# Kernel optimization log

Measured on AMD Instinct MI355X. Metric: run time of the kernel, lower is better.

## Reference

```python
import jax, jax.numpy as jnp
import numpy as np

B, N, C = 1, 6400, 256
NUM_CAMS, NUM_HEADS, NUM_LEVELS, NUM_POINTS = 6, 8, 3, 8
LVL_SHAPES = [(64, 176), (32, 88), (16, 44)]
IMG_H, IMG_W = 512, 1408


def setup_inputs():
    key = jax.random.key(0)
    ks = jax.random.split(key, 16)
    # Gaussian means in ego frame: depth z in [2,40]; x/y scaled so projections land in-image
    z = jax.random.uniform(ks[0], (B, N, 1), minval=2.0, maxval=40.0)
    xy = jax.random.uniform(ks[1], (B, N, 2), minval=-0.5, maxval=0.5)
    means = jnp.concatenate([xy[..., 0:1] * z * 0.8, xy[..., 1:2] * z * 0.4, z], -1)
    feature = jax.random.normal(ks[2], (B, N, C)) * 0.5
    feat0 = jax.random.normal(ks[3], (B * NUM_CAMS, C, 64, 176)) * 0.5
    feat1 = jax.random.normal(ks[4], (B * NUM_CAMS, C, 32, 88)) * 0.5
    feat2 = jax.random.normal(ks[5], (B * NUM_CAMS, C, 16, 44)) * 0.5
    cam2ego = jnp.tile(jnp.eye(4), (B, NUM_CAMS, 1, 1))
    cam2ego = cam2ego.at[..., :3, 3].set(jax.random.uniform(ks[6], (B, NUM_CAMS, 3), minval=-0.5, maxval=0.5))
    intrins = jnp.tile(jnp.array([[500., 0., 704.], [0., 500., 256.], [0., 0., 1.]]), (B, NUM_CAMS, 1, 1))
    post_rots = jnp.tile(jnp.eye(3), (B, NUM_CAMS, 1, 1))
    post_trans = jnp.concatenate([jax.random.uniform(ks[7], (B, NUM_CAMS, 2), minval=-30., maxval=30.),
                                  jnp.zeros((B, NUM_CAMS, 1))], -1)
    # deformable-attn style bias init for sampling offsets (as in init_weights)
    thetas = np.arange(NUM_HEADS) * (2.0 * np.pi / NUM_HEADS)
    grid = np.stack([np.cos(thetas), np.sin(thetas)], -1)
    grid = grid / np.abs(grid).max(-1, keepdims=True)
    grid = np.tile(grid.reshape(NUM_HEADS, 1, 1, 2), (1, NUM_LEVELS, NUM_POINTS, 1))
    grid = grid * (np.arange(NUM_POINTS) + 1).reshape(1, 1, NUM_POINTS, 1)
    b_off = jnp.asarray(grid.reshape(-1), jnp.float32)
    W_off = jax.random.normal(ks[8], (C, NUM_HEADS * NUM_LEVELS * NUM_POINTS * 2)) * 0.01
    W_attn = jax.random.normal(ks[9], (C, NUM_HEADS * NUM_LEVELS * NUM_POINTS)) * 0.02
    b_attn = jnp.zeros((NUM_HEADS * NUM_LEVELS * NUM_POINTS,))
    W_val = jax.random.normal(ks[10], (C, C)) * (1.0 / np.sqrt(C))
    b_val = jnp.zeros((C,))
    W_out = jax.random.normal(ks[11], (C, C)) * (1.0 / np.sqrt(C))
    b_out = jnp.zeros((C,))
    cams_embeds = jax.random.normal(ks[12], (NUM_CAMS, C))
    level_embeds = jax.random.normal(ks[13], (NUM_LEVELS, C))
    ln_g = jnp.ones((C,))
    ln_b = jnp.zeros((C,))
    return dict(means=means, feature=feature, feat0=feat0, feat1=feat1, feat2=feat2,
                cam2ego=cam2ego, intrins=intrins, post_rots=post_rots, post_trans=post_trans,
                W_off=W_off, b_off=b_off, W_attn=W_attn, b_attn=b_attn, W_val=W_val, b_val=b_val,
                W_out=W_out, b_out=b_out, cams_embeds=cams_embeds, level_embeds=level_embeds,
                ln_g=ln_g, ln_b=ln_b, img_h=IMG_H, img_w=IMG_W)


def _msda(value, shapes, loc, attn):
    # Multi-scale deformable attention (matches multi_scale_deformable_attn_pytorch,
    # i.e. grid_sample bilinear, align_corners=False, zero padding).
    # value [Bc,S,H,D]; loc [Bc,Nq,H,L,P,2] in [0,1]; attn [Bc,Nq,H,L,P]
    Bc, S, Hh, D = value.shape
    Nq, P = loc.shape[1], loc.shape[4]
    out = jnp.zeros((Bc, Hh, Nq, D), value.dtype)
    start = 0
    for lvl, (h, w) in enumerate(shapes):
        v = value[:, start:start + h * w].transpose(0, 2, 1, 3)  # [Bc,H,h*w,D]
        l = loc[:, :, :, lvl]                                    # [Bc,Nq,H,P,2]
        x = l[..., 0] * w - 0.5  # align_corners=False pixel coords
        y = l[..., 1] * h - 0.5
        x0 = jnp.floor(x)
        y0 = jnp.floor(y)
        tx = x - x0
        ty = y - y0
        a = attn[:, :, :, lvl]                                   # [Bc,Nq,H,P]
        def samp(xi, yi, wgt):
            valid = (xi >= 0) & (xi <= w - 1) & (yi >= 0) & (yi <= h - 1)
            idx = (jnp.clip(yi, 0, h - 1) * w + jnp.clip(xi, 0, w - 1)).astype(jnp.int32)
            idx = idx.transpose(0, 2, 1, 3).reshape(Bc, Hh, Nq * P)
            g = jnp.take_along_axis(v, idx[..., None], axis=2)   # [Bc,H,Nq*P,D]
            coef = wgt * jnp.where(valid, 1.0, 0.0).astype(v.dtype) * a
            return g * coef.transpose(0, 2, 1, 3).reshape(Bc, Hh, Nq * P, 1)
        acc = (samp(x0, y0, (1 - tx) * (1 - ty)) + samp(x0 + 1, y0, tx * (1 - ty))
               + samp(x0, y0 + 1, (1 - tx) * ty) + samp(x0 + 1, y0 + 1, tx * ty))
        out = out + acc.reshape(Bc, Hh, Nq, P, D).sum(3)
        start += h * w
    return out.transpose(0, 2, 1, 3).reshape(Bc, Nq, Hh * D)


def reference(means, feature, feat0, feat1, feat2, cam2ego, intrins, post_rots, post_trans,
              W_off, b_off, W_attn, b_attn, W_val, b_val, W_out, b_out,
              cams_embeds, level_embeds, ln_g, ln_b, img_h, img_w):
    Bq, Nq, Cc = feature.shape
    D = Cc // NUM_HEADS
    # --- project reference points into each camera (project_reference_points) ---
    mh = jnp.concatenate([means, jnp.ones((Bq, Nq, 1), means.dtype)], -1)      # [B,N,4]
    means_cam = jnp.einsum('bcij,bnj->bcni', jnp.linalg.inv(cam2ego), mh)[..., :3]
    means_img = jnp.einsum('bcij,bcnj->bcni', intrins, means_cam)              # [B,cams,N,3]
    mi = jnp.concatenate([means_img[..., :2] / (means_img[..., 2:] + 1e-4), means_img[..., 2:]], -1)
    mi = jnp.einsum('bcij,bcnj->bcni', post_rots, mi) + post_trans[:, :, None, :]
    coor = mi[..., :2] / jnp.array([img_w, img_h], feature.dtype)              # [B,cams,N,2]
    depth = mi[..., 2]
    mask = ((depth > 0.01) & (coor[..., 0] > 0.) & (coor[..., 0] < 1.)
            & (coor[..., 1] > 0.) & (coor[..., 1] < 1.))                        # [B,cams,N]
    # --- per-query sampling offsets / attention weights (shared across cameras) ---
    offsets = (feature @ W_off + b_off).reshape(Bq, Nq, NUM_HEADS, NUM_LEVELS, NUM_POINTS, 2)
    attn = jax.nn.softmax((feature @ W_attn + b_attn).reshape(Bq, Nq, NUM_HEADS, NUM_LEVELS * NUM_POINTS), -1)
    attn = attn.reshape(Bq, Nq, NUM_HEADS, NUM_LEVELS, NUM_POINTS)
    # --- flatten multi-level feats + cam/level embeds, value projection ---
    feats = (feat0, feat1, feat2)
    shapes = [(f.shape[2], f.shape[3]) for f in feats]
    flat = []
    for lvl, f in enumerate(feats):
        h, w = shapes[lvl]
        fl = f.reshape(Bq, NUM_CAMS, Cc, h * w)
        fl = fl + cams_embeds[None, :, :, None] + level_embeds[lvl][None, None, :, None]
        flat.append(fl)
    value = jnp.concatenate(flat, -1).transpose(0, 1, 3, 2).reshape(Bq * NUM_CAMS, -1, Cc)
    value = (value @ W_val + b_val).reshape(Bq * NUM_CAMS, -1, NUM_HEADS, D)
    # --- sampling locations per camera ---
    norm = jnp.array([[w, h] for (h, w) in shapes], feature.dtype)             # [L,2] = (W_l,H_l)
    loc = coor[:, :, :, None, None, None, :] + offsets[:, None] / norm[None, None, None, None, :, None, :]
    loc = loc.reshape(Bq * NUM_CAMS, Nq, NUM_HEADS, NUM_LEVELS, NUM_POINTS, 2)
    attn_bc = jnp.broadcast_to(attn[:, None], (Bq, NUM_CAMS, Nq, NUM_HEADS, NUM_LEVELS, NUM_POINTS))
    attn_bc = attn_bc.reshape(Bq * NUM_CAMS, Nq, NUM_HEADS, NUM_LEVELS, NUM_POINTS)
    out = _msda(value, shapes, loc, attn_bc).reshape(Bq, NUM_CAMS, Nq, Cc)
    # --- mask-weighted combine over cameras (mathematically equals the rebatch/scatter) ---
    mf = mask.astype(feature.dtype)
    slots = (out * mf[..., None]).sum(1) / jnp.maximum(mf.sum(1), 1.0)[..., None]
    slots = slots @ W_out + b_out
    x = slots + feature  # dropout is identity at inference
    mu = jnp.mean(x, -1, keepdims=True)
    var = jnp.mean((x - mu) ** 2, -1, keepdims=True)
    return (x - mu) / jnp.sqrt(var + 1e-5) * ln_g + ln_b
```

## Files before the change

kernel.cpp:

```cpp
#include <hip/hip_runtime.h>
#include <hip/hip_bf16.h>

typedef __bf16 bf16;
typedef __attribute__((ext_vector_type(4))) float f32x4;
typedef __attribute__((ext_vector_type(8))) bf16 bf16x8;
typedef __attribute__((ext_vector_type(2))) bf16 bf16x2;

#define NCAMS 6
#define NQ 6400
#define CH 256
#define NH 8
#define NL 3
#define NP 8
#define S_TOT 14784

#if __has_builtin(__builtin_amdgcn_fdot2_f32_bf16) && __has_builtin(__builtin_amdgcn_perm)
#define MSDA_DOT2 1
#else
#define MSDA_DOT2 0
#endif

__global__ __launch_bounds__(256) void k_prep(
    const float* __restrict__ means, const float* __restrict__ cam2ego,
    const float* __restrict__ intrins, const float* __restrict__ post_rots,
    const float* __restrict__ post_trans, const int* __restrict__ img_h,
    const int* __restrict__ img_w,
    const float* __restrict__ W_val, const float* __restrict__ W_off,
    const float* __restrict__ W_attn, const float* __restrict__ W_out,
    float* __restrict__ coor, float* __restrict__ maskf,
    bf16* __restrict__ Wvp, bf16* __restrict__ Woap, bf16* __restrict__ Wop)
{
    int bid = blockIdx.x;
    if (bid < 150) {
        int idx = bid * 256 + threadIdx.x;
        if (idx >= NCAMS * NQ) return;
        int cam = idx / NQ, n = idx % NQ;
        float mx = means[n*3+0], my = means[n*3+1], mz = means[n*3+2];
        const float* M = cam2ego + cam*16;
        float R[3][3], t[3];
        #pragma unroll
        for (int r = 0; r < 3; r++) {
            #pragma unroll
            for (int c = 0; c < 3; c++) R[r][c] = M[r*4+c];
            t[r] = M[r*4+3];
        }
        float dx = mx - t[0], dy = my - t[1], dz = mz - t[2];
        float xc = R[0][0]*dx + R[1][0]*dy + R[2][0]*dz;
        float yc = R[0][1]*dx + R[1][1]*dy + R[2][1]*dz;
        float zc = R[0][2]*dx + R[1][2]*dy + R[2][2]*dz;
        const float* K = intrins + cam*9;
        float ix = K[0]*xc + K[1]*yc + K[2]*zc;
        float iy = K[3]*xc + K[4]*yc + K[5]*zc;
        float iz = K[6]*xc + K[7]*yc + K[8]*zc;
        float px = ix / (iz + 1e-4f), py = iy / (iz + 1e-4f), pz = iz;
        const float* P = post_rots + cam*9;
        const float* T = post_trans + cam*3;
        float vx = P[0]*px + P[1]*py + P[2]*pz + T[0];
        float vy = P[3]*px + P[4]*py + P[5]*pz + T[1];
        float vz = P[6]*px + P[7]*py + P[8]*pz + T[2];
        float cx = vx / (float)img_w[0];
        float cy = vy / (float)img_h[0];
        bool ok = (vz > 0.01f) && (cx > 0.f) && (cx < 1.f) && (cy > 0.f) && (cy < 1.f);
        coor[idx*2+0] = cx;
        coor[idx*2+1] = cy;
        maskf[idx] = ok ? 1.f : 0.f;
        return;
    }
    int flat = (bid - 150) * 256 + threadIdx.x;
    if (flat < 8192) {
        int kc = flat >> 10, rem = flat & 1023;
        int nf = rem >> 6, lane = rem & 63;
        int q = lane >> 4, col = nf*16 + (lane & 15);
        bf16x8 v;
        #pragma unroll
        for (int j = 0; j < 8; j++) v[j] = (bf16)W_val[(size_t)(kc*32 + q*8 + j)*256 + col];
        *reinterpret_cast<bf16x8*>(Wvp + (size_t)flat*8) = v;
    } else if (flat < 26624) {
        int f2 = flat - 8192;
        int kc = f2 / (36*64), rem = f2 % (36*64);
        int nf = rem >> 6, lane = rem & 63;
        int q = lane >> 4, col = nf*16 + (lane & 15);
        bf16x8 v;
        #pragma unroll
        for (int j = 0; j < 8; j++) {
            int k = kc*32 + q*8 + j;
            float x = (col < 384) ? W_off[(size_t)k*384 + col] : W_attn[(size_t)k*192 + (col-384)];
            v[j] = (bf16)x;
        }
        *reinterpret_cast<bf16x8*>(Woap + (size_t)f2*8) = v;
    } else if (flat < 34816) {
        int f3 = flat - 26624;
        int kc = f3 >> 10, rem = f3 & 1023;
        int nf = rem >> 6, lane = rem & 63;
        int q = lane >> 4, col = nf*16 + (lane & 15);
        bf16x8 v;
        #pragma unroll
        for (int j = 0; j < 8; j++) v[j] = (bf16)W_out[(size_t)(kc*32 + q*8 + j)*256 + col];
        *reinterpret_cast<bf16x8*>(Wop + (size_t)f3*8) = v;
    }
}

__global__ __launch_bounds__(256) void k_offattn2(
    const float* __restrict__ feature, const bf16* __restrict__ Woap,
    const float* __restrict__ b_off, const float* __restrict__ b_attn,
    float* __restrict__ offs, bf16* __restrict__ attn_out)
{
    __shared__ float lg[16][200];
    int t = threadIdx.x, lane = t & 63, w = t >> 6;
    int q = lane >> 4, r16 = lane & 15;
    int n0 = blockIdx.x * 16;

    f32x4 acc[9];
    #pragma unroll
    for (int i = 0; i < 9; i++) acc[i] = (f32x4){0.f,0.f,0.f,0.f};

    const float* arow = feature + (size_t)(n0 + r16)*CH;
    for (int kc = 0; kc < 8; kc++) {
        f32x4 a0 = *reinterpret_cast<const f32x4*>(arow + kc*32 + q*8);
        f32x4 a1 = *reinterpret_cast<const f32x4*>(arow + kc*32 + q*8 + 4);
        bf16x8 afr;
        #pragma unroll
        for (int i = 0; i < 4; i++) { afr[i] = (bf16)a0[i]; afr[4+i] = (bf16)a1[i]; }
        #pragma unroll
        for (int nf9 = 0; nf9 < 9; nf9++) {
            bf16x8 bfr = *reinterpret_cast<const bf16x8*>(Woap + ((size_t)(kc*36 + w*9 + nf9)*64 + lane)*8);
            acc[nf9] = __builtin_amdgcn_mfma_f32_16x16x32_bf16(afr, bfr, acc[nf9], 0, 0, 0);
        }
    }
    #pragma unroll
    for (int nf9 = 0; nf9 < 9; nf9++) {
        int nfg = w*9 + nf9;
        int nglob = nfg*16 + r16;
        if (nfg < 24) {
            float bias = b_off[nglob];
            #pragma unroll
            for (int r = 0; r < 4; r++)
                offs[(size_t)(n0 + q*4 + r)*384 + nglob] = acc[nf9][r] + bias;
        } else {
            int la = nglob - 384;
            float bias = b_attn[la];
            #pragma unroll
            for (int r = 0; r < 4; r++)
                lg[q*4 + r][la] = acc[nf9][r] + bias;
        }
    }
    __syncthreads();
    if (t < 128) {
        int m = t >> 3, h = t & 7;
        const float* L = &lg[m][h*24];
        float mx = -1e30f;
        #pragma unroll
        for (int j = 0; j < 24; j++) mx = fmaxf(mx, L[j]);
        float e[24]; float s = 0.f;
        #pragma unroll
        for (int j = 0; j < 24; j++) { e[j] = __expf(L[j] - mx); s += e[j]; }
        float inv = 1.f / s;
        #pragma unroll
        for (int j = 0; j < 24; j++) attn_out[(size_t)(n0+m)*192 + h*24 + j] = (bf16)(e[j]*inv);
    }
}

__global__ __launch_bounds__(256) void k_valproj(
    const float* __restrict__ f0, const float* __restrict__ f1, const float* __restrict__ f2,
    const float* __restrict__ cams_embeds, const float* __restrict__ level_embeds,
    const bf16* __restrict__ Wvp, const float* __restrict__ b_val, bf16* __restrict__ value)
{
    __shared__ alignas(16) bf16 A[64][48];
    __shared__ alignas(16) bf16 Cst[16][256];
    int bi = blockIdx.x;
    int cam = bi / 231, mb = bi % 231;
    int lvl, local0, HW;
    const float* fp;
    if (mb < 176)      { lvl = 0; local0 = mb*64;        fp = f0; HW = 11264; }
    else if (mb < 220) { lvl = 1; local0 = (mb-176)*64;  fp = f1; HW = 2816;  }
    else               { lvl = 2; local0 = (mb-220)*64;  fp = f2; HW = 704;   }
    int pos0 = (lvl == 0 ? 0 : (lvl == 1 ? 11264 : 14080)) + local0;
    const float* featbase = fp + (size_t)cam*CH*HW + local0;

    int t = threadIdx.x;
    int lane = t & 63, w = t >> 6;
    int kk = t >> 3;
    int m8 = (t & 7) * 8;
    int q = lane >> 4, r16 = lane & 15;

    f32x4 acc[4][4];
    #pragma unroll
    for (int i = 0; i < 4; i++)
        #pragma unroll
        for (int j = 0; j < 4; j++) acc[i][j] = (f32x4){0.f,0.f,0.f,0.f};

    for (int kc = 0; kc < 8; kc++) {
        __syncthreads();
        int kg = kc*32 + kk;
        float e = cams_embeds[cam*CH + kg] + level_embeds[lvl*CH + kg];
        f32x4 v0 = *reinterpret_cast<const f32x4*>(featbase + (size_t)kg*HW + m8);
        f32x4 v1 = *reinterpret_cast<const f32x4*>(featbase + (size_t)kg*HW + m8 + 4);
        #pragma unroll
        for (int i = 0; i < 4; i++) A[m8+i][kk]   = (bf16)(v0[i] + e);
        #pragma unroll
        for (int i = 0; i < 4; i++) A[m8+4+i][kk] = (bf16)(v1[i] + e);
        __syncthreads();

        bf16x8 bfr[4];
        #pragma unroll
        for (int nf = 0; nf < 4; nf++) {
            int nfg = w*4 + nf;
            bfr[nf] = *reinterpret_cast<const bf16x8*>(Wvp + ((size_t)(kc*16 + nfg)*64 + lane)*8);
        }
        #pragma unroll
        for (int mf = 0; mf < 4; mf++) {
            bf16x8 afr = *reinterpret_cast<const bf16x8*>(&A[mf*16 + r16][q*8]);
            #pragma unroll
            for (int nf = 0; nf < 4; nf++)
                acc[mf][nf] = __builtin_amdgcn_mfma_f32_16x16x32_bf16(afr, bfr[nf], acc[mf][nf], 0, 0, 0);
        }
    }
    int orow = t >> 4;
    int ocol = (t & 15) * 16;
    int ohead = ocol >> 5, och = ocol & 31;
    #pragma unroll
    for (int mf = 0; mf < 4; mf++) {
        __syncthreads();
        #pragma unroll
        for (int nf = 0; nf < 4; nf++) {
            int c = w*64 + nf*16 + r16;
            float bv = b_val[c];
            #pragma unroll
            for (int r = 0; r < 4; r++)
                Cst[q*4 + r][c] = (bf16)(acc[mf][nf][r] + bv);
        }
        __syncthreads();
        int srow = pos0 + mf*16 + orow;
        bf16* dst = value + ((size_t)(cam*NH + ohead)*S_TOT + srow)*32 + och;
        const f32x4* src = reinterpret_cast<const f32x4*>(&Cst[orow][ocol]);
        f32x4 x0 = src[0], x1 = src[1];
        reinterpret_cast<f32x4*>(dst)[0] = x0;
        reinterpret_cast<f32x4*>(dst)[1] = x1;
    }
}

__global__ __launch_bounds__(256) void k_msda(
    const float* __restrict__ coor, const float* __restrict__ offs,
    const bf16* __restrict__ attn, const bf16* __restrict__ value,
    const float* __restrict__ maskf, float* __restrict__ slots)
{
#if MSDA_DOT2
    __shared__ uint2 s_w[4][48];
#else
    __shared__ f32x4 s_w[4][48];
#endif
    __shared__ int4  s_o[4][48];
    int wv = threadIdx.x >> 6;
    int lane = threadIdx.x & 63;
    int n = blockIdx.x;
    int h0 = wv * 2;
    int p = lane >> 3, k = lane & 7;
    int kb = k * 8;

    float oxr = 0.f, oyr = 0.f, awr = 0.f;
    int smm = h0*24 + lane;
    if (lane < 48) {
        float2 o2 = *reinterpret_cast<const float2*>(offs + (size_t)n*384 + smm*2);
        oxr = o2.x; oyr = o2.y;
        awr = (float)attn[(size_t)n*192 + smm];
    }

    f32x4 acc[2];
    acc[0] = (f32x4){0.f, 0.f, 0.f, 0.f};
    acc[1] = (f32x4){0.f, 0.f, 0.f, 0.f};

    const char* vbyte = (const char*)value;

    for (int cam = 0; cam < NCAMS; cam++) {
        if (maskf[cam*NQ + n] == 0.f) continue;
        float cx = coor[(cam*NQ + n)*2 + 0];
        float cy = coor[(cam*NQ + n)*2 + 1];

        if (lane < 48) {
            int hl = lane / 24;
            int r = lane - hl*24;
            int lvl = r >> 3;
            int h = h0 + hl;
            int wi   = (lvl == 0) ? 176 : ((lvl == 1) ? 88 : 44);
            int hi   = (lvl == 0) ? 64  : ((lvl == 1) ? 32 : 16);
            int base = (lvl == 0) ? 0   : ((lvl == 1) ? 11264 : 14080);
            float x = cx*(float)wi + oxr - 0.5f;
            float y = cy*(float)hi + oyr - 0.5f;
            float xf = floorf(x), yf = floorf(y);
            float tx = x - xf, ty = y - yf;
            float wm1x = (float)(wi-1), wm1y = (float)(hi-1);
            bool vx0 = (xf >= 0.f)      && (xf <= wm1x);
            bool vx1 = (xf+1.f >= 0.f)  && (xf+1.f <= wm1x);
            bool vy0 = (yf >= 0.f)      && (yf <= wm1y);
            bool vy1 = (yf+1.f >= 0.f)  && (yf+1.f <= wm1y);
            int x0 = (int)fminf(fmaxf(xf,      0.f), wm1x);
            int x1 = (int)fminf(fmaxf(xf+1.f,  0.f), wm1x);
            int y0 = (int)fminf(fmaxf(yf,      0.f), wm1y);
            int y1 = (int)fminf(fmaxf(yf+1.f,  0.f), wm1y);
            float w00 = (1.f-tx)*(1.f-ty)*awr * ((vx0 && vy0) ? 1.f : 0.f);
            float w10 = tx*(1.f-ty)*awr       * ((vx1 && vy0) ? 1.f : 0.f);
            float w01 = (1.f-tx)*ty*awr       * ((vx0 && vy1) ? 1.f : 0.f);
            float w11 = tx*ty*awr             * ((vx1 && vy1) ? 1.f : 0.f);
            int rowb = (cam*NH + h)*S_TOT + base;
            int r0 = rowb + y0*wi, r1 = rowb + y1*wi;
#if MSDA_DOT2
            bf16x2 wa; wa[0] = (bf16)w00; wa[1] = (bf16)w10;
            bf16x2 wb; wb[0] = (bf16)w01; wb[1] = (bf16)w11;
            s_w[wv][lane] = make_uint2(__builtin_bit_cast(unsigned, wa),
                                       __builtin_bit_cast(unsigned, wb));
#else
            s_w[wv][lane] = (f32x4){w00, w10, w01, w11};
#endif
            s_o[wv][lane] = make_int4((r0 + x0)*64, (r0 + x1)*64, (r1 + x0)*64, (r1 + x1)*64);
        }

        #pragma unroll
        for (int hl = 0; hl < 2; hl++) {
            #pragma unroll
            for (int lvl = 0; lvl < 3; lvl++) {
                int mml = hl*24 + lvl*8 + p;
                int4  o4 = s_o[wv][mml];
#if MSDA_DOT2
                uint2 wp = s_w[wv][mml];
                bf16x2 wa = __builtin_bit_cast(bf16x2, wp.x);
                bf16x2 wb = __builtin_bit_cast(bf16x2, wp.y);
                uint2 d00 = *reinterpret_cast<const uint2*>(vbyte + (o4.x + kb));
                uint2 d10 = *reinterpret_cast<const uint2*>(vbyte + (o4.y + kb));
                uint2 d01 = *reinterpret_cast<const uint2*>(vbyte + (o4.z + kb));
                uint2 d11 = *reinterpret_cast<const uint2*>(vbyte + (o4.w + kb));
                unsigned a0p = __builtin_amdgcn_perm(d10.x, d00.x, 0x05040100u);
                unsigned a1p = __builtin_amdgcn_perm(d10.x, d00.x, 0x07060302u);
                unsigned a2p = __builtin_amdgcn_perm(d10.y, d00.y, 0x05040100u);
                unsigned a3p = __builtin_amdgcn_perm(d10.y, d00.y, 0x07060302u);
                unsigned b0p = __builtin_amdgcn_perm(d11.x, d01.x, 0x05040100u);
                unsigned b1p = __builtin_amdgcn_perm(d11.x, d01.x, 0x07060302u);
                unsigned b2p = __builtin_amdgcn_perm(d11.y, d01.y, 0x05040100u);
                unsigned b3p = __builtin_amdgcn_perm(d11.y, d01.y, 0x07060302u);
                acc[hl][0] = __builtin_amdgcn_fdot2_f32_bf16(__builtin_bit_cast(bf16x2, a0p), wa, acc[hl][0], false);
                acc[hl][1] = __builtin_amdgcn_fdot2_f32_bf16(__builtin_bit_cast(bf16x2, a1p), wa, acc[hl][1], false);
                acc[hl][2] = __builtin_amdgcn_fdot2_f32_bf16(__builtin_bit_cast(bf16x2, a2p), wa, acc[hl][2], false);
                acc[hl][3] = __builtin_amdgcn_fdot2_f32_bf16(__builtin_bit_cast(bf16x2, a3p), wa, acc[hl][3], false);
                acc[hl][0] = __builtin_amdgcn_fdot2_f32_bf16(__builtin_bit_cast(bf16x2, b0p), wb, acc[hl][0], false);
                acc[hl][1] = __builtin_amdgcn_fdot2_f32_bf16(__builtin_bit_cast(bf16x2, b1p), wb, acc[hl][1], false);
                acc[hl][2] = __builtin_amdgcn_fdot2_f32_bf16(__builtin_bit_cast(bf16x2, b2p), wb, acc[hl][2], false);
                acc[hl][3] = __builtin_amdgcn_fdot2_f32_bf16(__builtin_bit_cast(bf16x2, b3p), wb, acc[hl][3], false);
#else
                f32x4 w4 = s_w[wv][mml];
                uint2 d00 = *reinterpret_cast<const uint2*>(vbyte + (o4.x + kb));
                uint2 d10 = *reinterpret_cast<const uint2*>(vbyte + (o4.y + kb));
                uint2 d01 = *reinterpret_cast<const uint2*>(vbyte + (o4.z + kb));
                uint2 d11 = *reinterpret_cast<const uint2*>(vbyte + (o4.w + kb));
                acc[hl][0] = fmaf(__uint_as_float(d00.x << 16),          w4.x, acc[hl][0]);
                acc[hl][1] = fmaf(__uint_as_float(d00.x & 0xffff0000u),  w4.x, acc[hl][1]);
                acc[hl][2] = fmaf(__uint_as_float(d00.y << 16),          w4.x, acc[hl][2]);
                acc[hl][3] = fmaf(__uint_as_float(d00.y & 0xffff0000u),  w4.x, acc[hl][3]);
                acc[hl][0] = fmaf(__uint_as_float(d10.x << 16),          w4.y, acc[hl][0]);
                acc[hl][1] = fmaf(__uint_as_float(d10.x & 0xffff0000u),  w4.y, acc[hl][1]);
                acc[hl][2] = fmaf(__uint_as_float(d10.y << 16),          w4.y, acc[hl][2]);
                acc[hl][3] = fmaf(__uint_as_float(d10.y & 0xffff0000u),  w4.y, acc[hl][3]);
                acc[hl][0] = fmaf(__uint_as_float(d01.x << 16),          w4.z, acc[hl][0]);
                acc[hl][1] = fmaf(__uint_as_float(d01.x & 0xffff0000u),  w4.z, acc[hl][1]);
                acc[hl][2] = fmaf(__uint_as_float(d01.y << 16),          w4.z, acc[hl][2]);
                acc[hl][3] = fmaf(__uint_as_float(d01.y & 0xffff0000u),  w4.z, acc[hl][3]);
                acc[hl][0] = fmaf(__uint_as_float(d11.x << 16),          w4.w, acc[hl][0]);
                acc[hl][1] = fmaf(__uint_as_float(d11.x & 0xffff0000u),  w4.w, acc[hl][1]);
                acc[hl][2] = fmaf(__uint_as_float(d11.y << 16),          w4.w, acc[hl][2]);
                acc[hl][3] = fmaf(__uint_as_float(d11.y & 0xffff0000u),  w4.w, acc[hl][3]);
#endif
            }
        }
    }

    #pragma unroll
    for (int hl = 0; hl < 2; hl++)
        #pragma unroll
        for (int i = 0; i < 4; i++) {
            acc[hl][i] += __shfl_xor(acc[hl][i], 8);
            acc[hl][i] += __shfl_xor(acc[hl][i], 16);
            acc[hl][i] += __shfl_xor(acc[hl][i], 32);
        }
    if (p == 0) {
        #pragma unroll
        for (int hl = 0; hl < 2; hl++)
            *reinterpret_cast<f32x4*>(slots + (size_t)n*CH + (h0+hl)*32 + k*4) = acc[hl];
    }
}

__global__ __launch_bounds__(256) void k_final2(
    const float* __restrict__ slots, const float* __restrict__ maskf,
    const bf16* __restrict__ Wop, const float* __restrict__ b_out,
    const float* __restrict__ feature, const float* __restrict__ ln_g,
    const float* __restrict__ ln_b, float* __restrict__ out)
{
    __shared__ float yb[16][264];
    int t = threadIdx.x, lane = t & 63, w = t >> 6;
    int q = lane >> 4, r16 = lane & 15;
    int n0 = blockIdx.x * 16;

    float msum = 0.f;
    #pragma unroll
    for (int cam = 0; cam < NCAMS; cam++) msum += maskf[cam*NQ + n0 + r16];
    float inv = 1.f / fmaxf(msum, 1.f);

    f32x4 acc[4];
    #pragma unroll
    for (int i = 0; i < 4; i++) acc[i] = (f32x4){0.f,0.f,0.f,0.f};

    const float* srow = slots + (size_t)(n0 + r16)*CH;
    for (int kc = 0; kc < 8; kc++) {
        f32x4 a0 = *reinterpret_cast<const f32x4*>(srow + kc*32 + q*8);
        f32x4 a1 = *reinterpret_cast<const f32x4*>(srow + kc*32 + q*8 + 4);
        bf16x8 afr;
        #pragma unroll
        for (int i = 0; i < 4; i++) { afr[i] = (bf16)(a0[i]*inv); afr[4+i] = (bf16)(a1[i]*inv); }
        #pragma unroll
        for (int nf = 0; nf < 4; nf++) {
            bf16x8 bfr = *reinterpret_cast<const bf16x8*>(Wop + ((size_t)(kc*16 + w*4 + nf)*64 + lane)*8);
            acc[nf] = __builtin_amdgcn_mfma_f32_16x16x32_bf16(afr, bfr, acc[nf], 0, 0, 0);
        }
    }
    #pragma unroll
    for (int nf = 0; nf < 4; nf++) {
        int c = (w*4 + nf)*16 + r16;
        float bias = b_out[c];
        #pragma unroll
        for (int r = 0; r < 4; r++) {
            int m = q*4 + r;
            yb[m][c] = acc[nf][r] + bias + feature[(size_t)(n0+m)*CH + c];
        }
    }
    __syncthreads();
    int row = t >> 4, l16 = t & 15;
    int c0 = l16 * 16;
    float s = 0.f, s2 = 0.f;
    #pragma unroll
    for (int j = 0; j < 16; j++) {
        float v = yb[row][c0 + j];
        s += v; s2 += v*v;
    }
    #pragma unroll
    for (int off = 1; off < 16; off <<= 1) {
        s  += __shfl_xor(s, off);
        s2 += __shfl_xor(s2, off);
    }
    float mu = s / 256.f;
    float rsig = rsqrtf(s2 / 256.f - mu*mu + 1e-5f);
    float* orow = out + (size_t)(n0 + row)*CH + c0;
    #pragma unroll
    for (int j4 = 0; j4 < 4; j4++) {
        f32x4 o;
        #pragma unroll
        for (int i = 0; i < 4; i++) {
            int c = c0 + j4*4 + i;
            o[i] = (yb[row][c] - mu) * rsig * ln_g[c] + ln_b[c];
        }
        *reinterpret_cast<f32x4*>(orow + j4*4) = o;
    }
}

extern "C" void kernel_launch(void* const* d_in, const int* in_sizes, int n_in,
                              void* d_out, int out_size, void* d_ws, size_t ws_size,
                              hipStream_t stream)
{
    const float* means       = (const float*)d_in[0];
    const float* feature     = (const float*)d_in[1];
    const float* feat0       = (const float*)d_in[2];
    const float* feat1       = (const float*)d_in[3];
    const float* feat2       = (const float*)d_in[4];
    const float* cam2ego     = (const float*)d_in[5];
    const float* intrins     = (const float*)d_in[6];
    const float* post_rots   = (const float*)d_in[7];
    const float* post_trans  = (const float*)d_in[8];
    const float* W_off       = (const float*)d_in[9];
    const float* b_off       = (const float*)d_in[10];
    const float* W_attn      = (const float*)d_in[11];
    const float* b_attn      = (const float*)d_in[12];
    const float* W_val       = (const float*)d_in[13];
    const float* b_val       = (const float*)d_in[14];
    const float* W_out       = (const float*)d_in[15];
    const float* b_out       = (const float*)d_in[16];
    const float* cams_embeds = (const float*)d_in[17];
    const float* level_embeds= (const float*)d_in[18];
    const float* ln_g        = (const float*)d_in[19];
    const float* ln_b        = (const float*)d_in[20];
    const int*   img_h       = (const int*)d_in[21];
    const int*   img_w       = (const int*)d_in[22];

    char* ws = (char*)d_ws;
    float* coor  = (float*)(ws + 0);
    float* maskf = (float*)(ws + 307200);
    float* offs  = (float*)(ws + 460800);
    bf16*  attn  = (bf16*) (ws + 10291200);
    bf16*  Wvp   = (bf16*) (ws + 12748800);
    bf16*  Woap  = (bf16*) (ws + 12879872);
    bf16*  Wop   = (bf16*) (ws + 13174784);
    float* slots = (float*)(ws + 13305856);
    bf16*  value = (bf16*) (ws + 19859456);
    if (ws_size < 65275904u) return;

    k_prep    <<<286, 256, 0, stream>>>(means, cam2ego, intrins, post_rots, post_trans,
                                        img_h, img_w, W_val, W_off, W_attn, W_out,
                                        coor, maskf, Wvp, Woap, Wop);
    k_offattn2<<<400, 256, 0, stream>>>(feature, Woap, b_off, b_attn, offs, attn);
    k_valproj <<<1386, 256, 0, stream>>>(feat0, feat1, feat2, cams_embeds, level_embeds, Wvp, b_val, value);
    k_msda    <<<6400, 256, 0, stream>>>(coor, offs, attn, value, maskf, slots);
    k_final2  <<<400, 256, 0, stream>>>(slots, maskf, Wop, b_out, feature, ln_g, ln_b, (float*)d_out);
}
```

Baseline: 322.6 us.

## Precompute all camera sampling params up front and widen per-lane value loads

The MSDA kernel now computes bilinear offsets and weights for all 6 cameras, 8 heads and 192 points in one block-wide pass into shared memory, followed by a single barrier. Previously each wave recomputed them per camera with only 48 active lanes. The mask is folded into the attention weight instead of skipping the camera, so masked cameras are now gathered with zero weight, which is extra memory traffic. The gather loop maps lanes as 2 heads x 8 points x 4 channel groups, so each lane issues 16-byte loads over 8 channels instead of 8-byte loads over 4, and a shorter shuffle reduction follows.

```diff
diff --git a/kernel.cpp b/kernel.cpp
--- a/kernel.cpp
+++ b/kernel.cpp
@@ -244,145 +244,176 @@
     const bf16* __restrict__ attn, const bf16* __restrict__ value,
     const float* __restrict__ maskf, float* __restrict__ slots)
 {
+    __shared__ int4  s_o[NCAMS*192];
 #if MSDA_DOT2
-    __shared__ uint2 s_w[4][48];
+    __shared__ uint2 s_w[NCAMS*192];
 #else
-    __shared__ f32x4 s_w[4][48];
+    __shared__ f32x4 s_w[NCAMS*192];
 #endif
-    __shared__ int4  s_o[4][48];
-    int wv = threadIdx.x >> 6;
-    int lane = threadIdx.x & 63;
     int n = blockIdx.x;
-    int h0 = wv * 2;
-    int p = lane >> 3, k = lane & 7;
-    int kb = k * 8;
-
-    float oxr = 0.f, oyr = 0.f, awr = 0.f;
-    int smm = h0*24 + lane;
-    if (lane < 48) {
-        float2 o2 = *reinterpret_cast<const float2*>(offs + (size_t)n*384 + smm*2);
-        oxr = o2.x; oyr = o2.y;
-        awr = (float)attn[(size_t)n*192 + smm];
-    }
-
-    f32x4 acc[2];
-    acc[0] = (f32x4){0.f, 0.f, 0.f, 0.f};
-    acc[1] = (f32x4){0.f, 0.f, 0.f, 0.f};
-
-    const char* vbyte = (const char*)value;
-
-    for (int cam = 0; cam < NCAMS; cam++) {
-        if (maskf[cam*NQ + n] == 0.f) continue;
+    int t = threadIdx.x;
+
+    for (int it = t; it < NCAMS*192; it += 256) {
+        int cam = it / 192;
+        int r   = it - cam*192;
+        int hh  = r / 24;
+        int rr  = r - hh*24;
+        int lvl = rr >> 3;
+
+        float mk = maskf[cam*NQ + n];
         float cx = coor[(cam*NQ + n)*2 + 0];
         float cy = coor[(cam*NQ + n)*2 + 1];
-
-        if (lane < 48) {
-            int hl = lane / 24;
-            int r = lane - hl*24;
-            int lvl = r >> 3;
-            int h = h0 + hl;
-            int wi   = (lvl == 0) ? 176 : ((lvl == 1) ? 88 : 44);
-            int hi   = (lvl == 0) ? 64  : ((lvl == 1) ? 32 : 16);
-            int base = (lvl == 0) ? 0   : ((lvl == 1) ? 11264 : 14080);
-            float x = cx*(float)wi + oxr - 0.5f;
-            float y = cy*(float)hi + oyr - 0.5f;
-            float xf = floorf(x), yf = floorf(y);
-            float tx = x - xf, ty = y - yf;
-            float wm1x = (float)(wi-1), wm1y = (float)(hi-1);
-            bool vx0 = (xf >= 0.f)      && (xf <= wm1x);
-            bool vx1 = (xf+1.f >= 0.f)  && (xf+1.f <= wm1x);
-            bool vy0 = (yf >= 0.f)      && (yf <= wm1y);
-            bool vy1 = (yf+1.f >= 0.f)  && (yf+1.f <= wm1y);
-            int x0 = (int)fminf(fmaxf(xf,      0.f), wm1x);
-            int x1 = (int)fminf(fmaxf(xf+1.f,  0.f), wm1x);
-            int y0 = (int)fminf(fmaxf(yf,      0.f), wm1y);
-            int y1 = (int)fminf(fmaxf(yf+1.f,  0.f), wm1y);
-            float w00 = (1.f-tx)*(1.f-ty)*awr * ((vx0 && vy0) ? 1.f : 0.f);
-            float w10 = tx*(1.f-ty)*awr       * ((vx1 && vy0) ? 1.f : 0.f);
-            float w01 = (1.f-tx)*ty*awr       * ((vx0 && vy1) ? 1.f : 0.f);
-            float w11 = tx*ty*awr             * ((vx1 && vy1) ? 1.f : 0.f);
-            int rowb = (cam*NH + h)*S_TOT + base;
-            int r0 = rowb + y0*wi, r1 = rowb + y1*wi;
+        float2 o2 = *reinterpret_cast<const float2*>(offs + (size_t)n*384 + r*2);
+        float aw = (float)attn[(size_t)n*192 + r] * mk;
+
+        int wi   = (lvl == 0) ? 176 : ((lvl == 1) ? 88 : 44);
+        int hi   = (lvl == 0) ? 64  : ((lvl == 1) ? 32 : 16);
+        int base = (lvl == 0) ? 0   : ((lvl == 1) ? 11264 : 14080);
+
+        float x = cx*(float)wi + o2.x - 0.5f;
+        float y = cy*(float)hi + o2.y - 0.5f;
+        float xf = floorf(x), yf = floorf(y);
+        float tx = x - xf, ty = y - yf;
+        float wm1x = (float)(wi-1), wm1y = (float)(hi-1);
+        bool vx0 = (xf >= 0.f)      && (xf <= wm1x);
+        bool vx1 = (xf+1.f >= 0.f)  && (xf+1.f <= wm1x);
+        bool vy0 = (yf >= 0.f)      && (yf <= wm1y);
+        bool vy1 = (yf+1.f >= 0.f)  && (yf+1.f <= wm1y);
+        int x0 = (int)fminf(fmaxf(xf,      0.f), wm1x);
+        int x1 = (int)fminf(fmaxf(xf+1.f,  0.f), wm1x);
+        int y0 = (int)fminf(fmaxf(yf,      0.f), wm1y);
+        int y1 = (int)fminf(fmaxf(yf+1.f,  0.f), wm1y);
+        float w00 = (1.f-tx)*(1.f-ty)*aw * ((vx0 && vy0) ? 1.f : 0.f);
+        float w10 = tx*(1.f-ty)*aw       * ((vx1 && vy0) ? 1.f : 0.f);
+        float w01 = (1.f-tx)*ty*aw       * ((vx0 && vy1) ? 1.f : 0.f);
+        float w11 = tx*ty*aw             * ((vx1 && vy1) ? 1.f : 0.f);
+        int rowb = (cam*NH + hh)*S_TOT + base;
+        int r0 = rowb + y0*wi, r1 = rowb + y1*wi;
+        s_o[it] = make_int4((r0 + x0)*64, (r0 + x1)*64, (r1 + x0)*64, (r1 + x1)*64);
 #if MSDA_DOT2
-            bf16x2 wa; wa[0] = (bf16)w00; wa[1] = (bf16)w10;
-            bf16x2 wb; wb[0] = (bf16)w01; wb[1] = (bf16)w11;
-            s_w[wv][lane] = make_uint2(__builtin_bit_cast(unsigned, wa),
-                                       __builtin_bit_cast(unsigned, wb));
+        bf16x2 wa; wa[0] = (bf16)w00; wa[1] = (bf16)w10;
+        bf16x2 wb; wb[0] = (bf16)w01; wb[1] = (bf16)w11;
+        s_w[it] = make_uint2(__builtin_bit_cast(unsigned, wa),
+                             __builtin_bit_cast(unsigned, wb));
 #else
-            s_w[wv][lane] = (f32x4){w00, w10, w01, w11};
+        s_w[it] = (f32x4){w00, w10, w01, w11};
 #endif
-            s_o[wv][lane] = make_int4((r0 + x0)*64, (r0 + x1)*64, (r1 + x0)*64, (r1 + x1)*64);
-        }
-
-        #pragma unroll
-        for (int hl = 0; hl < 2; hl++) {
-            #pragma unroll
-            for (int lvl = 0; lvl < 3; lvl++) {
-                int mml = hl*24 + lvl*8 + p;
-                int4  o4 = s_o[wv][mml];
+    }
+    __syncthreads();
+
+    int lane = t & 63, wv = t >> 6;
+    int hl = lane >> 5;
+    int p  = (lane >> 2) & 7;
+    int k2 = lane & 3;
+    int hglob = wv*2 + hl;
+    int kb = k2 * 16;
+    int ibase = hglob*24 + p;
+
+    f32x4 acc0 = (f32x4){0.f,0.f,0.f,0.f};
+    f32x4 acc1 = (f32x4){0.f,0.f,0.f,0.f};
+    const char* vbyte = (const char*)value;
+
+    #pragma unroll 2
+    for (int cam = 0; cam < NCAMS; cam++) {
+        #pragma unroll
+        for (int lvl = 0; lvl < 3; lvl++) {
+            int it = cam*192 + ibase + lvl*8;
+            int4  o4 = s_o[it];
 #if MSDA_DOT2
-                uint2 wp = s_w[wv][mml];
-                bf16x2 wa = __builtin_bit_cast(bf16x2, wp.x);
-                bf16x2 wb = __builtin_bit_cast(bf16x2, wp.y);
-                uint2 d00 = *reinterpret_cast<const uint2*>(vbyte + (o4.x + kb));
-                uint2 d10 = *reinterpret_cast<const uint2*>(vbyte + (o4.y + kb));
-                uint2 d01 = *reinterpret_cast<const uint2*>(vbyte + (o4.z + kb));
-                uint2 d11 = *reinterpret_cast<const uint2*>(vbyte + (o4.w + kb));
-                unsigned a0p = __builtin_amdgcn_perm(d10.x, d00.x, 0x05040100u);
-                unsigned a1p = __builtin_amdgcn_perm(d10.x, d00.x, 0x07060302u);
-                unsigned a2p = __builtin_amdgcn_perm(d10.y, d00.y, 0x05040100u);
-                unsigned a3p = __builtin_amdgcn_perm(d10.y, d00.y, 0x07060302u);
-                unsigned b0p = __builtin_amdgcn_perm(d11.x, d01.x, 0x05040100u);
-                unsigned b1p = __builtin_amdgcn_perm(d11.x, d01.x, 0x07060302u);
-                unsigned b2p = __builtin_amdgcn_perm(d11.y, d01.y, 0x05040100u);
-                unsigned b3p = __builtin_amdgcn_perm(d11.y, d01.y, 0x07060302u);
-                acc[hl][0] = __builtin_amdgcn_fdot2_f32_bf16(__builtin_bit_cast(bf16x2, a0p), wa, acc[hl][0], false);
-                acc[hl][1] = __builtin_amdgcn_fdot2_f32_bf16(__builtin_bit_cast(bf16x2, a1p), wa, acc[hl][1], false);
-                acc[hl][2] = __builtin_amdgcn_fdot2_f32_bf16(__builtin_bit_cast(bf16x2, a2p), wa, acc[hl][2], false);
-                acc[hl][3] = __builtin_amdgcn_fdot2_f32_bf16(__builtin_bit_cast(bf16x2, a3p), wa, acc[hl][3], false);
-                acc[hl][0] = __builtin_amdgcn_fdot2_f32_bf16(__builtin_bit_cast(bf16x2, b0p), wb, acc[hl][0], false);
-                acc[hl][1] = __builtin_amdgcn_fdot2_f32_bf16(__builtin_bit_cast(bf16x2, b1p), wb, acc[hl][1], false);
-                acc[hl][2] = __builtin_amdgcn_fdot2_f32_bf16(__builtin_bit_cast(bf16x2, b2p), wb, acc[hl][2], false);
-                acc[hl][3] = __builtin_amdgcn_fdot2_f32_bf16(__builtin_bit_cast(bf16x2, b3p), wb, acc[hl][3], false);
+            uint2 wp = s_w[it];
+            bf16x2 wa = __builtin_bit_cast(bf16x2, wp.x);
+            bf16x2 wb = __builtin_bit_cast(bf16x2, wp.y);
+            uint4 d00 = *reinterpret_cast<const uint4*>(vbyte + (o4.x + kb));
+            uint4 d10 = *reinterpret_cast<const uint4*>(vbyte + (o4.y + kb));
+            uint4 d01 = *reinterpret_cast<const uint4*>(vbyte + (o4.z + kb));
+            uint4 d11 = *reinterpret_cast<const uint4*>(vbyte + (o4.w + kb));
+            unsigned a0 = __builtin_amdgcn_perm(d10.x, d00.x, 0x05040100u);
+            unsigned a1 = __builtin_amdgcn_perm(d10.x, d00.x, 0x07060302u);
+            unsigned a2 = __builtin_amdgcn_perm(d10.y, d00.y, 0x05040100u);
+            unsigned a3 = __builtin_amdgcn_perm(d10.y, d00.y, 0x07060302u);
+            unsigned a4 = __builtin_amdgcn_perm(d10.z, d00.z, 0x05040100u);
+            unsigned a5 = __builtin_amdgcn_perm(d10.z, d00.z, 0x07060302u);
+            unsigned a6 = __builtin_amdgcn_perm(d10.w, d00.w, 0x05040100u);
+            unsigned a7 = __builtin_amdgcn_perm(d10.w, d00.w, 0x07060302u);
+            acc0[0] = __builtin_amdgcn_fdot2_f32_bf16(__builtin_bit_cast(bf16x2, a0), wa, acc0[0], false);
+            acc0[1] = __builtin_amdgcn_fdot2_f32_bf16(__builtin_bit_cast(bf16x2, a1), wa, acc0[1], false);
+            acc0[2] = __builtin_amdgcn_fdot2_f32_bf16(__builtin_bit_cast(bf16x2, a2), wa, acc0[2], false);
+            acc0[3] = __builtin_amdgcn_fdot2_f32_bf16(__builtin_bit_cast(bf16x2, a3), wa, acc0[3], false);
+            acc1[0] = __builtin_amdgcn_fdot2_f32_bf16(__builtin_bit_cast(bf16x2, a4), wa, acc1[0], false);
+            acc1[1] = __builtin_amdgcn_fdot2_f32_bf16(__builtin_bit_cast(bf16x2, a5), wa, acc1[1], false);
+            acc1[2] = __builtin_amdgcn_fdot2_f32_bf16(__builtin_bit_cast(bf16x2, a6), wa, acc1[2], false);
+            acc1[3] = __builtin_amdgcn_fdot2_f32_bf16(__builtin_bit_cast(bf16x2, a7), wa, acc1[3], false);
+            unsigned b0 = __builtin_amdgcn_perm(d11.x, d01.x, 0x05040100u);
+            unsigned b1 = __builtin_amdgcn_perm(d11.x, d01.x, 0x07060302u);
+            unsigned b2 = __builtin_amdgcn_perm(d11.y, d01.y, 0x05040100u);
+            unsigned b3 = __builtin_amdgcn_perm(d11.y, d01.y, 0x07060302u);
+            unsigned b4 = __builtin_amdgcn_perm(d11.z, d01.z, 0x05040100u);
+            unsigned b5 = __builtin_amdgcn_perm(d11.z, d01.z, 0x07060302u);
+            unsigned b6 = __builtin_amdgcn_perm(d11.w, d01.w, 0x05040100u);
+            unsigned b7 = __builtin_amdgcn_perm(d11.w, d01.w, 0x07060302u);
+            acc0[0] = __builtin_amdgcn_fdot2_f32_bf16(__builtin_bit_cast(bf16x2, b0), wb, acc0[0], false);
+            acc0[1] = __builtin_amdgcn_fdot2_f32_bf16(__builtin_bit_cast(bf16x2, b1), wb, acc0[1], false);
+            acc0[2] = __builtin_amdgcn_fdot2_f32_bf16(__builtin_bit_cast(bf16x2, b2), wb, acc0[2], false);
+            acc0[3] = __builtin_amdgcn_fdot2_f32_bf16(__builtin_bit_cast(bf16x2, b3), wb, acc0[3], false);
+            acc1[0] = __builtin_amdgcn_fdot2_f32_bf16(__builtin_bit_cast(bf16x2, b4), wb, acc1[0], false);
+            acc1[1] = __builtin_amdgcn_fdot2_f32_bf16(__builtin_bit_cast(bf16x2, b5), wb, acc1[1], false);
+            acc1[2] = __builtin_amdgcn_fdot2_f32_bf16(__builtin_bit_cast(bf16x2, b6), wb, acc1[2], false);
+            acc1[3] = __builtin_amdgcn_fdot2_f32_bf16(__builtin_bit_cast(bf16x2, b7), wb, acc1[3], false);
 #else
-                f32x4 w4 = s_w[wv][mml];
-                uint2 d00 = *reinterpret_cast<const uint2*>(vbyte + (o4.x + kb));
-                uint2 d10 = *reinterpret_cast<const uint2*>(vbyte + (o4.y + kb));
-                uint2 d01 = *reinterpret_cast<const uint2*>(vbyte + (o4.z + kb));
-                uint2 d11 = *reinterpret_cast<const uint2*>(vbyte + (o4.w + kb));
-                acc[hl][0] = fmaf(__uint_as_float(d00.x << 16),          w4.x, acc[hl][0]);
-                acc[hl][1] = fmaf(__uint_as_float(d00.x & 0xffff0000u),  w4.x, acc[hl][1]);
-                acc[hl][2] = fmaf(__uint_as_float(d00.y << 16),          w4.x, acc[hl][2]);
-                acc[hl][3] = fmaf(__uint_as_float(d00.y & 0xffff0000u),  w4.x, acc[hl][3]);
-                acc[hl][0] = fmaf(__uint_as_float(d10.x << 16),          w4.y, acc[hl][0]);
-                acc[hl][1] = fmaf(__uint_as_float(d10.x & 0xffff0000u),  w4.y, acc[hl][1]);
-                acc[hl][2] = fmaf(__uint_as_float(d10.y << 16),          w4.y, acc[hl][2]);
-                acc[hl][3] = fmaf(__uint_as_float(d10.y & 0xffff0000u),  w4.y, acc[hl][3]);
-                acc[hl][0] = fmaf(__uint_as_float(d01.x << 16),          w4.z, acc[hl][0]);
-                acc[hl][1] = fmaf(__uint_as_float(d01.x & 0xffff0000u),  w4.z, acc[hl][1]);
-                acc[hl][2] = fmaf(__uint_as_float(d01.y << 16),          w4.z, acc[hl][2]);
-                acc[hl][3] = fmaf(__uint_as_float(d01.y & 0xffff0000u),  w4.z, acc[hl][3]);
-                acc[hl][0] = fmaf(__uint_as_float(d11.x << 16),          w4.w, acc[hl][0]);
-                acc[hl][1] = fmaf(__uint_as_float(d11.x & 0xffff0000u),  w4.w, acc[hl][1]);
-                acc[hl][2] = fmaf(__uint_as_float(d11.y << 16),          w4.w, acc[hl][2]);
-                acc[hl][3] = fmaf(__uint_as_float(d11.y & 0xffff0000u),  w4.w, acc[hl][3]);
+            f32x4 w4 = s_w[it];
+            uint4 d00 = *reinterpret_cast<const uint4*>(vbyte + (o4.x + kb));
+            uint4 d10 = *reinterpret_cast<const uint4*>(vbyte + (o4.y + kb));
+            uint4 d01 = *reinterpret_cast<const uint4*>(vbyte + (o4.z + kb));
+            uint4 d11 = *reinterpret_cast<const uint4*>(vbyte + (o4.w + kb));
+            acc0[0] = fmaf(__uint_as_float(d00.x << 16),         w4.x, acc0[0]);
+            acc0[1] = fmaf(__uint_as_float(d00.x & 0xffff0000u), w4.x, acc0[1]);
+            acc0[2] = fmaf(__uint_as_float(d00.y << 16),         w4.x, acc0[2]);
+            acc0[3] = fmaf(__uint_as_float(d00.y & 0xffff0000u), w4.x, acc0[3]);
+            acc1[0] = fmaf(__uint_as_float(d00.z << 16),         w4.x, acc1[0]);
+            acc1[1] = fmaf(__uint_as_float(d00.z & 0xffff0000u), w4.x, acc1[1]);
+            acc1[2] = fmaf(__uint_as_float(d00.w << 16),         w4.x, acc1[2]);
+            acc1[3] = fmaf(__uint_as_float(d00.w & 0xffff0000u), w4.x, acc1[3]);
+            acc0[0] = fmaf(__uint_as_float(d10.x << 16),         w4.y, acc0[0]);
+            acc0[1] = fmaf(__uint_as_float(d10.x & 0xffff0000u), w4.y, acc0[1]);
+            acc0[2] = fmaf(__uint_as_float(d10.y << 16),         w4.y, acc0[2]);
+            acc0[3] = fmaf(__uint_as_float(d10.y & 0xffff0000u), w4.y, acc0[3]);
+            acc1[0] = fmaf(__uint_as_float(d10.z << 16),         w4.y, acc1[0]);
+            acc1[1] = fmaf(__uint_as_float(d10.z & 0xffff0000u), w4.y, acc1[1]);
+            acc1[2] = fmaf(__uint_as_float(d10.w << 16),         w4.y, acc1[2]);
+            acc1[3] = fmaf(__uint_as_float(d10.w & 0xffff0000u), w4.y, acc1[3]);
+            acc0[0] = fmaf(__uint_as_float(d01.x << 16),         w4.z, acc0[0]);
+            acc0[1] = fmaf(__uint_as_float(d01.x & 0xffff0000u), w4.z, acc0[1]);
+            acc0[2] = fmaf(__uint_as_float(d01.y << 16),         w4.z, acc0[2]);
+            acc0[3] = fmaf(__uint_as_float(d01.y & 0xffff0000u), w4.z, acc0[3]);
+            acc1[0] = fmaf(__uint_as_float(d01.z << 16),         w4.z, acc1[0]);
+            acc1[1] = fmaf(__uint_as_float(d01.z & 0xffff0000u), w4.z, acc1[1]);
+            acc1[2] = fmaf(__uint_as_float(d01.w << 16),         w4.z, acc1[2]);
+            acc1[3] = fmaf(__uint_as_float(d01.w & 0xffff0000u), w4.z, acc1[3]);
+            acc0[0] = fmaf(__uint_as_float(d11.x << 16),         w4.w, acc0[0]);
+            acc0[1] = fmaf(__uint_as_float(d11.x & 0xffff0000u), w4.w, acc0[1]);
+            acc0[2] = fmaf(__uint_as_float(d11.y << 16),         w4.w, acc0[2]);
+            acc0[3] = fmaf(__uint_as_float(d11.y & 0xffff0000u), w4.w, acc0[3]);
+            acc1[0] = fmaf(__uint_as_float(d11.z << 16),         w4.w, acc1[0]);
+            acc1[1] = fmaf(__uint_as_float(d11.z & 0xffff0000u), w4.w, acc1[1]);
+            acc1[2] = fmaf(__uint_as_float(d11.w << 16),         w4.w, acc1[2]);
+            acc1[3] = fmaf(__uint_as_float(d11.w & 0xffff0000u), w4.w, acc1[3]);
 #endif
-            }
-        }
-    }
-
-    #pragma unroll
-    for (int hl = 0; hl < 2; hl++)
-        #pragma unroll
-        for (int i = 0; i < 4; i++) {
-            acc[hl][i] += __shfl_xor(acc[hl][i], 8);
-            acc[hl][i] += __shfl_xor(acc[hl][i], 16);
-            acc[hl][i] += __shfl_xor(acc[hl][i], 32);
-        }
+        }
+    }
+
+    #pragma unroll
+    for (int i = 0; i < 4; i++) {
+        acc0[i] += __shfl_xor(acc0[i], 4);
+        acc0[i] += __shfl_xor(acc0[i], 8);
+        acc0[i] += __shfl_xor(acc0[i], 16);
+        acc1[i] += __shfl_xor(acc1[i], 4);
+        acc1[i] += __shfl_xor(acc1[i], 8);
+        acc1[i] += __shfl_xor(acc1[i], 16);
+    }
     if (p == 0) {
-        #pragma unroll
-        for (int hl = 0; hl < 2; hl++)
-            *reinterpret_cast<f32x4*>(slots + (size_t)n*CH + (h0+hl)*32 + k*4) = acc[hl];
+        float* dst = slots + (size_t)n*CH + hglob*32 + k2*8;
+        *reinterpret_cast<f32x4*>(dst)     = acc0;
+        *reinterpret_cast<f32x4*>(dst + 4) = acc1;
     }
 }
 
```

After: 302.8 us. 6.1% less time.
